# Performance work log

Measured on AMD Instinct MI355X. Metric: run time of the kernel, lower is better.

Reference implementation:

```python
import jax, jax.numpy as jnp
import numpy as np

BN_EPS = 1e-5
KNN_K = 9
HEAD = 4


def _bn(x, gamma, beta, axis=1):
    # eval-mode BatchNorm with running_mean=0, running_var=1
    shape = [1] * x.ndim
    shape[axis] = -1
    scale = (gamma / jnp.sqrt(1.0 + BN_EPS)).reshape(shape)
    return x * scale + beta.reshape(shape)


def _conv1d(x, W, b):
    # 1x1 Conv1d == channel matmul; x: [B,C,N], W: [O,C], b: [O]
    return jnp.einsum('oc,bcn->bon', W, x) + b[None, :, None]


def _knn_idx(x, k):
    # x: [B,C,N] -> idx [B,N,k] of k nearest (incl. self)
    xx = jnp.sum(x * x, axis=1)                      # [B,N]
    inner = jnp.einsum('bcn,bcm->bnm', x, x)         # [B,N,N]
    neg_d = 2.0 * inner - xx[:, :, None] - xx[:, None, :]
    return jax.lax.top_k(neg_d, k)[1]


def _graph_feature(x, k):
    # x: [B,C,N] -> [B,2C,N,k]  (cat of center feature and center - neighbor)
    B, C, N = x.shape
    idx = _knn_idx(x, k)                             # [B,N,k]
    xt = jnp.transpose(x, (0, 2, 1))                 # [B,N,C]
    nbr = jax.vmap(lambda xb, ib: xb[ib])(xt, idx)   # [B,N,k,C]
    ctr = jnp.broadcast_to(xt[:, :, None, :], (B, N, k, C))
    feat = jnp.concatenate([ctr, ctr - nbr], axis=3)  # [B,N,k,2C]
    return jnp.transpose(feat, (0, 3, 1, 2))


def _dgcnn_max(x, w1, b1, g1, be1, w2, b2, g2, be2, k):
    # x: [B,C,N] -> [B,C,N]; two 1x1 convs + BN + ReLU then max over k
    ef = _graph_feature(x, k)                        # [B,2C,N,k]
    h = jnp.einsum('oc,bcnk->bonk', w1, ef) + b1[None, :, None, None]
    h = jax.nn.relu(_bn(h, g1, be1, axis=1))
    h = jnp.einsum('oc,bcnk->bonk', w2, h) + b2[None, :, None, None]
    h = jax.nn.relu(_bn(h, g2, be2, axis=1))
    return jnp.max(h, axis=-1)                       # [B,C,N]


def _attention(m1, m2, wq, bq, wk, bk, wv, bv, wmh, bmh, wc1, bc1, cg, cbe, wc2, bc2):
    B, C, N = m1.shape
    hd = C // HEAD
    q = _conv1d(m1, wq, bq).reshape(B, HEAD, hd, N)
    kk = _conv1d(m2, wk, bk).reshape(B, HEAD, hd, -1)
    v = _conv1d(m2, wv, bv).reshape(B, HEAD, hd, -1)
    score = jax.nn.softmax(jnp.einsum('bhdn,bhdm->bhnm', q, kk) / (float(hd) ** 0.5), axis=-1)
    add = jnp.einsum('bhnm,bhdm->bhdn', score, v).reshape(B, C, N)
    add = _conv1d(add, wmh, bmh)
    cat = jnp.concatenate([m1, add], axis=1)         # [B,2C,N]
    h = jax.nn.relu(_bn(_conv1d(cat, wc1, bc1), cg, cbe, axis=1))
    return m1 + _conv1d(h, wc2, bc2)


def setup_inputs() -> dict:
    key = jax.random.key(0)
    B, C, N = 4, 128, 2000
    ks = jax.random.split(key, 24)

    def w(k, shape, s=0.05):
        return jax.random.normal(k, shape, dtype=jnp.float32) * s

    inp = {
        'x': jax.random.normal(ks[0], (B, C, N, 1), dtype=jnp.float32),
        'y': jax.random.normal(ks[1], (B, C, N), dtype=jnp.float32),
        # DGCNN_MAX_Block conv params (two 1x1 Conv2d + BN)
        'dg_w1': w(ks[2], (C, 2 * C)), 'dg_b1': w(ks[3], (C,)),
        'dg_g1': jnp.ones((C,), jnp.float32), 'dg_be1': jnp.zeros((C,), jnp.float32),
        'dg_w2': w(ks[4], (C, C)), 'dg_b2': w(ks[5], (C,)),
        'dg_g2': jnp.ones((C,), jnp.float32), 'dg_be2': jnp.zeros((C,), jnp.float32),
        # AttentionPropagation params
        'wq': w(ks[6], (C, C)), 'bq': w(ks[7], (C,)),
        'wk': w(ks[8], (C, C)), 'bk': w(ks[9], (C,)),
        'wv': w(ks[10], (C, C)), 'bv': w(ks[11], (C,)),
        'wmh': w(ks[12], (C, C)), 'bmh': w(ks[13], (C,)),
        'wc1': w(ks[14], (2 * C, 2 * C)), 'bc1': w(ks[15], (2 * C,)),
        'cg': jnp.ones((2 * C,), jnp.float32), 'cbe': jnp.zeros((2 * C,), jnp.float32),
        'wc2': w(ks[16], (C, 2 * C)), 'bc2': w(ks[17], (C,)),
    }
    return inp


def reference(x, y, dg_w1, dg_b1, dg_g1, dg_be1, dg_w2, dg_b2, dg_g2, dg_be2,
              wq, bq, wk, bk, wv, bv, wmh, bmh, wc1, bc1, cg, cbe, wc2, bc2):
    feats = x[:, :, :, 0]                            # [B,C,N]
    agg = _dgcnn_max(feats, dg_w1, dg_b1, dg_g1, dg_be1,
                     dg_w2, dg_b2, dg_g2, dg_be2, KNN_K)
    out = _attention(agg, y, wq, bq, wk, bk, wv, bv, wmh, bmh,
                     wc1, bc1, cg, cbe, wc2, bc2)
    return out[:, :, :, None]                        # [B,C,N,1]
```

## Files before the change

### kernel.cpp

```cpp
#include <hip/hip_runtime.h>

#define BATCH 4
#define CH    128
#define NPTS  2000
#define KNN   9
#define NHEAD 4
#define HD    32
#define NHALF 1000

typedef unsigned short u16;
typedef __attribute__((ext_vector_type(4))) float f32x4;
typedef __attribute__((ext_vector_type(8))) short bf16x8;

#define OFF_XT    0
#define OFF_YT    1024000
#define OFF_PT    2048000
#define OFF_QT    3072000
#define OFF_AGG   4096000
#define OFF_MH    5120000
#define OFF_MISC  6144000
#define OFF_W1SUM (OFF_MISC)
#define OFF_W1B   (OFF_MISC+16384)
#define OFF_W2T   (OFF_MISC+32768)
#define OFF_ML0   (OFF_MISC+49152)
#define OFF_WC1T  (OFF_MISC+114688)
#define OFF_B1F   (OFF_MISC+212992)
#define OFF_B2F   (OFF_MISC+213120)
#define OFF_BC1F  (OFF_MISC+213248)
#define OFF_XX    (OFF_MISC+213504)
#define OFF_IDX   (OFF_MISC+221504)

__device__ __forceinline__ void bsplit(float v, u16& hi, u16& lo)
{
    unsigned u = __float_as_uint(v);
    unsigned h16 = (u + 0x7fffu + ((u >> 16) & 1u)) >> 16;
    float hf = __uint_as_float(h16 << 16);
    float lf = v - hf;
    unsigned ul = __float_as_uint(lf);
    hi = (u16)h16;
    lo = (u16)((ul + 0x7fffu + ((ul >> 16) & 1u)) >> 16);
}

__device__ __forceinline__ f32x4 mfma16(bf16x8 a, bf16x8 b, f32x4 c)
{
    return __builtin_amdgcn_mfma_f32_16x16x32_bf16(a, b, c, 0, 0, 0);
}

__global__ __launch_bounds__(256) void prep_kernel(
    const float* __restrict__ w1, const float* __restrict__ b1,
    const float* __restrict__ g1, const float* __restrict__ be1,
    const float* __restrict__ w2, const float* __restrict__ b2,
    const float* __restrict__ g2, const float* __restrict__ be2,
    const float* __restrict__ wc1, const float* __restrict__ bc1,
    const float* __restrict__ cg, const float* __restrict__ cbe,
    float* __restrict__ ws)
{
    int id = blockIdx.x * 256 + threadIdx.x;
    const float rs = rsqrtf(1.f + 1e-5f);
    if (id < 16384) {
        int o = id >> 7;
        int c = id & 127;
        float s1 = g1[o] * rs;
        ws[OFF_W1SUM + id] = (w1[o*256 + c] + w1[o*256 + 128 + c]) * s1;
        ws[OFF_W1B   + id] = w1[o*256 + 128 + c] * s1;
        ws[OFF_W2T   + id] = w2[id] * (g2[o] * rs);
    }
    {
        int o = id >> 8;
        ws[OFF_WC1T + id] = wc1[id] * (cg[o] * rs);
    }
    if (id < 128) {
        float s1 = g1[id] * rs, s2 = g2[id] * rs;
        ws[OFF_B1F + id] = b1[id]*s1 + be1[id];
        ws[OFF_B2F + id] = b2[id]*s2 + be2[id];
    }
    if (id < 256) {
        ws[OFF_BC1F + id] = bc1[id]*(cg[id]*rs) + cbe[id];
    }
}

__global__ __launch_bounds__(128) void transpose_split_kernel(
    const float* __restrict__ src, float* __restrict__ dst, float* __restrict__ xx,
    u16* __restrict__ H, u16* __restrict__ L)
{
    int blk = blockIdx.x; int b = blk / NPTS, n = blk % NPTS;
    int c = threadIdx.x;
    float v = src[((size_t)b*CH + c)*NPTS + n];
    size_t di = ((size_t)b*NPTS + n)*CH + c;
    dst[di] = v;
    u16 hi, lo;
    bsplit(v, hi, lo);
    H[di] = hi; L[di] = lo;
    __shared__ float red[128];
    red[c] = v*v;
    __syncthreads();
    for (int s = 64; s > 0; s >>= 1) { if (c < s) red[c] += red[c+s]; __syncthreads(); }
    if (c == 0) xx[b*NPTS + n] = red[0];
}

__global__ __launch_bounds__(128) void transpose_kernel(
    const float* __restrict__ src, float* __restrict__ dst)
{
    int blk = blockIdx.x; int b = blk / NPTS, n = blk % NPTS;
    int c = threadIdx.x;
    dst[((size_t)b*NPTS + n)*CH + c] = src[((size_t)b*CH + c)*NPTS + n];
}

__global__ __launch_bounds__(512) void knn8_kernel(
    const u16* __restrict__ XH, const u16* __restrict__ XL,
    const float* __restrict__ xx, int* __restrict__ idxOut)
{
    __shared__ float woutv[8][16][9];
    __shared__ int   wouti[8][16][9];
    int b = blockIdx.y;
    int q0 = blockIdx.x * 16;
    int tid = threadIdx.x;
    int wave = tid >> 6, lane = tid & 63;
    int lg = lane >> 4, lr = lane & 15;
    const float* xxb = xx + (size_t)b*NPTS;

    size_t qb = ((size_t)b*NPTS + q0 + lr)*128 + lg*8;
    bf16x8 qh[4], ql[4];
#pragma unroll
    for (int ch = 0; ch < 4; ch++) {
        qh[ch] = *(const bf16x8*)&XH[qb + ch*32];
        ql[ch] = *(const bf16x8*)&XL[qb + ch*32];
    }

    float vals[4][9]; int ids[4][9];
    float vmin[4]; int amin[4];
#pragma unroll
    for (int j = 0; j < 4; j++) {
#pragma unroll
        for (int k = 0; k < 9; k++) { vals[j][k] = -3.4e38f; ids[j][k] = -1; }
        vmin[j] = -3.4e38f; amin[j] = 0;
    }

    for (int t = wave; t < 125; t += 8) {
        size_t kb = ((size_t)b*NPTS + t*16 + lr)*128 + lg*8;
        bf16x8 fh[4], fl[4];
#pragma unroll
        for (int ch = 0; ch < 4; ch++) {
            fh[ch] = *(const bf16x8*)&XH[kb + ch*32];
            fl[ch] = *(const bf16x8*)&XL[kb + ch*32];
        }
        float xv = xxb[t*16 + lr];
        f32x4 acc = {0.f,0.f,0.f,0.f};
#pragma unroll
        for (int ch = 0; ch < 4; ch++) {
            acc = mfma16(qh[ch], fh[ch], acc);
            acc = mfma16(qh[ch], fl[ch], acc);
            acc = mfma16(ql[ch], fh[ch], acc);
            acc = mfma16(ql[ch], fl[ch], acc);
        }
        int cand = t*16 + lr;
#pragma unroll
        for (int j = 0; j < 4; j++) {
            float s = 2.f*acc[j] - xv;
            if (s > vmin[j]) {
#pragma unroll
                for (int k = 0; k < 9; k++) {
                    bool sel = (k == amin[j]);
                    vals[j][k] = sel ? s    : vals[j][k];
                    ids[j][k]  = sel ? cand : ids[j][k];
                }
                vmin[j] = vals[j][0]; amin[j] = 0;
#pragma unroll
                for (int k = 1; k < 9; k++) {
                    bool lt = vals[j][k] < vmin[j];
                    vmin[j] = lt ? vals[j][k] : vmin[j];
                    amin[j] = lt ? k : amin[j];
                }
            }
        }
    }

#pragma unroll
    for (int j = 0; j < 4; j++) {
        unsigned used = 0;
        for (int r = 0; r < 9; r++) {
            float bv = -3.4e38f; int bm = -1;
#pragma unroll
            for (int k = 0; k < 9; k++) {
                bool ok = !(used & (1u << k)) && (vals[j][k] > bv);
                bv = ok ? vals[j][k] : bv;
                bm = ok ? ids[j][k]  : bm;
            }
            float v = bv; int mi = bm;
#pragma unroll
            for (int off = 1; off < 16; off <<= 1) {
                float ov = __shfl_xor(v, off);
                int  omi = __shfl_xor(mi, off);
                if (ov > v || (ov == v && omi >= 0 && omi < mi)) { v = ov; mi = omi; }
            }
#pragma unroll
            for (int k = 0; k < 9; k++) {
                if (ids[j][k] == mi) used |= (1u << k);
            }
            if (lr == 0) { woutv[wave][lg*4+j][r] = v; wouti[wave][lg*4+j][r] = mi; }
        }
    }
    __syncthreads();

    if (tid < 16) {
        float v0 = woutv[0][tid][0], v1 = woutv[1][tid][0], v2 = woutv[2][tid][0], v3 = woutv[3][tid][0];
        float v4 = woutv[4][tid][0], v5 = woutv[5][tid][0], v6 = woutv[6][tid][0], v7 = woutv[7][tid][0];
        int   i0 = wouti[0][tid][0], i1 = wouti[1][tid][0], i2 = wouti[2][tid][0], i3 = wouti[3][tid][0];
        int   i4 = wouti[4][tid][0], i5 = wouti[5][tid][0], i6 = wouti[6][tid][0], i7 = wouti[7][tid][0];
        int   p0 = 1, p1 = 1, p2 = 1, p3 = 1, p4 = 1, p5 = 1, p6 = 1, p7 = 1;
        int* op = idxOut + ((size_t)b*NPTS + q0 + tid)*KNN;
        for (int r = 0; r < 9; r++) {
            int w = 0; float bv = v0; int bi = i0;
            if (v1 > bv || (v1 == bv && i1 < bi)) { w = 1; bv = v1; bi = i1; }
            if (v2 > bv || (v2 == bv && i2 < bi)) { w = 2; bv = v2; bi = i2; }
            if (v3 > bv || (v3 == bv && i3 < bi)) { w = 3; bv = v3; bi = i3; }
            if (v4 > bv || (v4 == bv && i4 < bi)) { w = 4; bv = v4; bi = i4; }
            if (v5 > bv || (v5 == bv && i5 < bi)) { w = 5; bv = v5; bi = i5; }
            if (v6 > bv || (v6 == bv && i6 < bi)) { w = 6; bv = v6; bi = i6; }
            if (v7 > bv || (v7 == bv && i7 < bi)) { w = 7; bv = v7; bi = i7; }
            op[r] = bi;
            if (w == 0)      { v0 = (p0 < 9) ? woutv[0][tid][p0] : -3.4e38f; i0 = (p0 < 9) ? wouti[0][tid][p0] : 0x7fffffff; p0++; }
            else if (w == 1) { v1 = (p1 < 9) ? woutv[1][tid][p1] : -3.4e38f; i1 = (p1 < 9) ? wouti[1][tid][p1] : 0x7fffffff; p1++; }
            else if (w == 2) { v2 = (p2 < 9) ? woutv[2][tid][p2] : -3.4e38f; i2 = (p2 < 9) ? wouti[2][tid][p2] : 0x7fffffff; p2++; }
            else if (w == 3) { v3 = (p3 < 9) ? woutv[3][tid][p3] : -3.4e38f; i3 = (p3 < 9) ? wouti[3][tid][p3] : 0x7fffffff; p3++; }
            else if (w == 4) { v4 = (p4 < 9) ? woutv[4][tid][p4] : -3.4e38f; i4 = (p4 < 9) ? wouti[4][tid][p4] : 0x7fffffff; p4++; }
            else if (w == 5) { v5 = (p5 < 9) ? woutv[5][tid][p5] : -3.4e38f; i5 = (p5 < 9) ? wouti[5][tid][p5] : 0x7fffffff; p5++; }
            else if (w == 6) { v6 = (p6 < 9) ? woutv[6][tid][p6] : -3.4e38f; i6 = (p6 < 9) ? wouti[6][tid][p6] : 0x7fffffff; p6++; }
            else             { v7 = (p7 < 9) ? woutv[7][tid][p7] : -3.4e38f; i7 = (p7 < 9) ? wouti[7][tid][p7] : 0x7fffffff; p7++; }
        }
    }
}

__global__ __launch_bounds__(128) void gemm_dual_kernel(
    const float* __restrict__ In, const float* __restrict__ Wa, const float* __restrict__ Wb,
    const float* __restrict__ ba, const float* __restrict__ bb,
    float* __restrict__ OutA, float* __restrict__ OutB)
{
    __shared__ float in_lds[8][128];
    int row0 = blockIdx.x * 8, tid = threadIdx.x;
    const float* src = In + (size_t)row0 * 128;
    for (int i = tid; i < 1024; i += 128) ((float*)in_lds)[i] = src[i];
    __syncthreads();
    float accA[8], accB[8];
    float bA = ba ? ba[tid] : 0.f, bB = bb ? bb[tid] : 0.f;
#pragma unroll
    for (int j = 0; j < 8; j++) { accA[j] = bA; accB[j] = bB; }
    const float4* wra = (const float4*)(Wa + (size_t)tid * 128);
    const float4* wrb = (const float4*)(Wb + (size_t)tid * 128);
#pragma unroll 4
    for (int c4 = 0; c4 < 32; c4++) {
        float4 wa = wra[c4], wb = wrb[c4];
#pragma unroll
        for (int j = 0; j < 8; j++) {
            float4 xi = ((const float4*)&in_lds[j][0])[c4];
            accA[j] += xi.x*wa.x + xi.y*wa.y + xi.z*wa.z + xi.w*wa.w;
            accB[j] += xi.x*wb.x + xi.y*wb.y + xi.z*wb.z + xi.w*wb.w;
        }
    }
#pragma unroll
    for (int j = 0; j < 8; j++) {
        OutA[(size_t)(row0 + j)*128 + tid] = accA[j];
        OutB[(size_t)(row0 + j)*128 + tid] = accB[j];
    }
}

__global__ __launch_bounds__(128) void gemm_kv_kernel(
    const float* __restrict__ In, const float* __restrict__ Wa, const float* __restrict__ Wb,
    const float* __restrict__ ba, const float* __restrict__ bb,
    u16* __restrict__ KHo, u16* __restrict__ KLo,
    u16* __restrict__ VTHo, u16* __restrict__ VTLo)
{
    __shared__ float in_lds[8][128];
    int row0 = blockIdx.x * 8, tid = threadIdx.x;
    const float* src = In + (size_t)row0 * 128;
    for (int i = tid; i < 1024; i += 128) ((float*)in_lds)[i] = src[i];
    __syncthreads();
    float accA[8], accB[8];
    float bA = ba[tid], bB = bb[tid];
#pragma unroll
    for (int j = 0; j < 8; j++) { accA[j] = bA; accB[j] = bB; }
    const float4* wra = (const float4*)(Wa + (size_t)tid * 128);
    const float4* wrb = (const float4*)(Wb + (size_t)tid * 128);
#pragma unroll 4
    for (int c4 = 0; c4 < 32; c4++) {
        float4 wa = wra[c4], wb = wrb[c4];
#pragma unroll
        for (int j = 0; j < 8; j++) {
            float4 xi = ((const float4*)&in_lds[j][0])[c4];
            accA[j] += xi.x*wa.x + xi.y*wa.y + xi.z*wa.z + xi.w*wa.w;
            accB[j] += xi.x*wb.x + xi.y*wb.y + xi.z*wb.z + xi.w*wb.w;
        }
    }
    int b = row0 / NPTS, n0 = row0 % NPTS;
#pragma unroll
    for (int j = 0; j < 8; j++) {
        u16 hh, ll;
        bsplit(accA[j], hh, ll);
        size_t ko = (size_t)(row0 + j)*128 + tid;
        KHo[ko] = hh; KLo[ko] = ll;
        bsplit(accB[j], hh, ll);
        size_t vo = ((size_t)b*128 + tid)*NPTS + n0 + j;
        VTHo[vo] = hh; VTLo[vo] = ll;
    }
}

__global__ __launch_bounds__(128) void gemm_q_kernel(
    const float* __restrict__ In, const float* __restrict__ Wt, const float* __restrict__ bias,
    u16* __restrict__ H, u16* __restrict__ L)
{
    __shared__ float in_lds[8][128];
    int row0 = blockIdx.x * 8, tid = threadIdx.x;
    const float* src = In + (size_t)row0 * 128;
    for (int i = tid; i < 1024; i += 128) ((float*)in_lds)[i] = src[i];
    __syncthreads();
    float acc[8];
    float b = bias[tid];
#pragma unroll
    for (int j = 0; j < 8; j++) acc[j] = b;
    const float4* wrow = (const float4*)(Wt + (size_t)tid * 128);
#pragma unroll 4
    for (int c4 = 0; c4 < 32; c4++) {
        float4 w = wrow[c4];
#pragma unroll
        for (int j = 0; j < 8; j++) {
            float4 xi = ((const float4*)&in_lds[j][0])[c4];
            acc[j] += xi.x*w.x + xi.y*w.y + xi.z*w.z + xi.w*w.w;
        }
    }
#pragma unroll
    for (int j = 0; j < 8; j++) {
        u16 hh, ll;
        bsplit(acc[j], hh, ll);
        size_t o = (size_t)(row0 + j)*128 + tid;
        H[o] = hh; L[o] = ll;
    }
}

template<int CIN, int COUT, bool RELU, bool TRANSOUT, bool HASRES, bool CONCAT>
__global__ __launch_bounds__(COUT) void gemmT_kernel(
    const float* __restrict__ In, const float* __restrict__ In2,
    const float* __restrict__ Wt, const float* __restrict__ bias,
    const float* __restrict__ Res, float* __restrict__ Out)
{
    __shared__ float in_lds[8][CIN];
    int row0 = blockIdx.x * 8, tid = threadIdx.x;
    if (!CONCAT) {
        const float* src = In + (size_t)row0 * CIN;
        for (int i = tid; i < 8*CIN; i += COUT) ((float*)in_lds)[i] = src[i];
    } else {
        for (int i = tid; i < 8*128; i += COUT) {
            int j = i >> 7, c = i & 127;
            in_lds[j][c]       = In [(size_t)(row0 + j)*128 + c];
            in_lds[j][128 + c] = In2[(size_t)(row0 + j)*128 + c];
        }
    }
    __syncthreads();
    float acc[8];
    float b = bias ? bias[tid] : 0.f;
#pragma unroll
    for (int j = 0; j < 8; j++) acc[j] = b;
    const float4* wrow = (const float4*)(Wt + (size_t)tid * CIN);
#pragma unroll 4
    for (int c4 = 0; c4 < CIN/4; c4++) {
        float4 w = wrow[c4];
#pragma unroll
        for (int j = 0; j < 8; j++) {
            float4 xi = ((const float4*)&in_lds[j][0])[c4];
            acc[j] += xi.x*w.x + xi.y*w.y + xi.z*w.z + xi.w*w.w;
        }
    }
#pragma unroll
    for (int j = 0; j < 8; j++) {
        float v = acc[j];
        if (RELU) v = fmaxf(v, 0.f);
        size_t row = row0 + j;
        if (HASRES) v += Res[row*COUT + tid];
        if (!TRANSOUT) {
            Out[row*COUT + tid] = v;
        } else {
            int b_ = (int)(row / NPTS), n_ = (int)(row % NPTS);
            Out[((size_t)b_*COUT + tid)*NPTS + n_] = v;
        }
    }
}

__global__ __launch_bounds__(128) void edgeconv_kernel(
    const float* __restrict__ Pt, const float* __restrict__ Qt,
    const int* __restrict__ idx, const float* __restrict__ W2t,
    const float* __restrict__ b2f, float* __restrict__ Agg)
{
    int blk = blockIdx.x; int b = blk / NPTS, n = blk % NPTS;
    int o = threadIdx.x;
    __shared__ float r[9][128];
    __shared__ int mk[9];
    if (o < 9) mk[o] = idx[((size_t)b*NPTS + n)*KNN + o];
    __syncthreads();
    float p = Pt[((size_t)b*NPTS + n)*128 + o];
#pragma unroll
    for (int k = 0; k < 9; k++) {
        float q = Qt[((size_t)b*NPTS + mk[k])*128 + o];
        r[k][o] = fmaxf(p - q, 0.f);
    }
    __syncthreads();
    float acc[9];
#pragma unroll
    for (int k = 0; k < 9; k++) acc[k] = 0.f;
    const float4* w2row = (const float4*)(W2t + (size_t)o * 128);
#pragma unroll 2
    for (int c4 = 0; c4 < 32; c4++) {
        float4 w = w2row[c4];
#pragma unroll
        for (int k = 0; k < 9; k++) {
            float4 rv = ((const float4*)&r[k][0])[c4];
            acc[k] += rv.x*w.x + rv.y*w.y + rv.z*w.z + rv.w*w.w;
        }
    }
    float bb = b2f[o];
    float vmax = -3.4e38f;
#pragma unroll
    for (int k = 0; k < 9; k++) vmax = fmaxf(vmax, fmaxf(acc[k] + bb, 0.f));
    Agg[((size_t)b*NPTS + n)*128 + o] = vmax;
}

#define PSTR 72
__global__ __launch_bounds__(256) void attn_mfma_kernel(
    const u16* __restrict__ QH, const u16* __restrict__ QL,
    const u16* __restrict__ KH, const u16* __restrict__ KL,
    const u16* __restrict__ VTH, const u16* __restrict__ VTL,
    float* __restrict__ O0, float* __restrict__ O1,
    float* __restrict__ ML0, float* __restrict__ ML1)
{
    __shared__ alignas(16) u16 Ph[4][16][PSTR];
    __shared__ alignas(16) u16 Pl[4][16][PSTR];
    int b = blockIdx.z, h = blockIdx.y;
    int split = blockIdx.x & 1, qt = blockIdx.x >> 1;
    int wave = threadIdx.x >> 6, lane = threadIdx.x & 63;
    int lg = lane >> 4, lr = lane & 15;
    int q0 = qt * 64 + wave * 16;
    if (q0 >= NPTS) return;
    int kstart = split * NHALF, kend = kstart + NHALF;
    float* Op = split ? O1 : O0;
    float* ml = split ? ML1 : ML0;

    size_t qb = ((size_t)b*NPTS + q0 + lr)*128 + h*32 + lg*8;
    const bf16x8 qh = *(const bf16x8*)&QH[qb];
    const bf16x8 ql = *(const bf16x8*)&QL[qb];

    f32x4 o0 = {0.f,0.f,0.f,0.f}, o1 = {0.f,0.f,0.f,0.f};
    float mrun[4], lsum[4];
#pragma unroll
    for (int r = 0; r < 4; r++) { mrun[r] = -3.0e38f; lsum[r] = 0.f; }
    const float sc = 0.17677669529663687f;
    int shsrc = ((lr >> 2) << 4) | (lr & 3);

    for (int ks = kstart; ks < kend; ks += 32) {
        int k0i = ks + lr;      bool vk0 = k0i < kend; if (k0i > kend-1) k0i = kend-1;
        int k1i = ks + 16 + lr; bool vk1 = k1i < kend; if (k1i > kend-1) k1i = kend-1;
        size_t kb0 = ((size_t)b*NPTS + k0i)*128 + h*32 + lg*8;
        size_t kb1 = ((size_t)b*NPTS + k1i)*128 + h*32 + lg*8;
        bf16x8 k0h = *(const bf16x8*)&KH[kb0];
        bf16x8 k0l = *(const bf16x8*)&KL[kb0];
        bf16x8 k1h = *(const bf16x8*)&KH[kb1];
        bf16x8 k1l = *(const bf16x8*)&KL[kb1];
        f32x4 s0 = {0.f,0.f,0.f,0.f}, s1 = {0.f,0.f,0.f,0.f};
        s0 = mfma16(qh, k0h, s0);
        s0 = mfma16(qh, k0l, s0);
        s0 = mfma16(ql, k0h, s0);
        s1 = mfma16(qh, k1h, s1);
        s1 = mfma16(qh, k1l, s1);
        s1 = mfma16(ql, k1h, s1);
        float mx[4];
#pragma unroll
        for (int r = 0; r < 4; r++) {
            float a  = vk0 ? s0[r]*sc : -3.0e38f;
            float a2 = vk1 ? s1[r]*sc : -3.0e38f;
            s0[r] = a; s1[r] = a2;
            mx[r] = fmaxf(a, a2);
        }
#pragma unroll
        for (int off = 1; off < 16; off <<= 1) {
#pragma unroll
            for (int r = 0; r < 4; r++) mx[r] = fmaxf(mx[r], __shfl_xor(mx[r], off));
        }
        float e0[4], e1[4], rsu[4], sca[4];
#pragma unroll
        for (int r = 0; r < 4; r++) {
            float mn = fmaxf(mrun[r], mx[r]);
            sca[r] = __expf(mrun[r] - mn);
            mrun[r] = mn;
            e0[r] = __expf(s0[r] - mn);
            e1[r] = __expf(s1[r] - mn);
            rsu[r] = e0[r] + e1[r];
        }
#pragma unroll
        for (int off = 1; off < 16; off <<= 1) {
#pragma unroll
            for (int r = 0; r < 4; r++) rsu[r] += __shfl_xor(rsu[r], off);
        }
#pragma unroll
        for (int r = 0; r < 4; r++) lsum[r] = lsum[r]*sca[r] + rsu[r];
#pragma unroll
        for (int r = 0; r < 4; r++) {
            u16 h0, w0, h1, w1;
            bsplit(e0[r], h0, w0);
            bsplit(e1[r], h1, w1);
            int qr = lg*4 + r;
            Ph[wave][qr][lr]      = h0;
            Pl[wave][qr][lr]      = w0;
            Ph[wave][qr][16 + lr] = h1;
            Pl[wave][qr][16 + lr] = w1;
        }
        float scsel = (lr & 2) ? ((lr & 1) ? sca[3] : sca[2])
                               : ((lr & 1) ? sca[1] : sca[0]);
        float osc = __shfl(scsel, shsrc);
#pragma unroll
        for (int r = 0; r < 4; r++) { o0[r] *= osc; o1[r] *= osc; }
        int cb = ks + lg*8; if (cb > kend-8) cb = kend-8;
        bf16x8 pbh = *(const bf16x8*)&Ph[wave][lr][lg*8];
        bf16x8 pbl = *(const bf16x8*)&Pl[wave][lr][lg*8];
        size_t vb = ((size_t)b*128 + h*32 + lr)*NPTS + cb;
        bf16x8 v0h = *(const bf16x8*)&VTH[vb];
        bf16x8 v0l = *(const bf16x8*)&VTL[vb];
        bf16x8 v1h = *(const bf16x8*)&VTH[vb + 16*NPTS];
        bf16x8 v1l = *(const bf16x8*)&VTL[vb + 16*NPTS];
        o0 = mfma16(v0h, pbh, o0);
        o0 = mfma16(v0l, pbh, o0);
        o0 = mfma16(v0h, pbl, o0);
        o1 = mfma16(v1h, pbh, o1);
        o1 = mfma16(v1l, pbh, o1);
        o1 = mfma16(v1h, pbl, o1);
    }
    if (lr == 0) {
#pragma unroll
        for (int r = 0; r < 4; r++) {
            size_t mo = (((size_t)b*NHEAD + h)*NPTS + q0 + lg*4 + r)*2;
            ml[mo]   = mrun[r];
            ml[mo+1] = lsum[r];
        }
    }
    int q = q0 + lr;
    size_t ob = ((size_t)b*NPTS + q)*128 + h*32;
#pragma unroll
    for (int r = 0; r < 4; r++) {
        Op[ob + lg*4 + r]      = o0[r];
        Op[ob + 16 + lg*4 + r] = o1[r];
    }
}

__global__ __launch_bounds__(256) void attn_merge_kernel(
    const float* __restrict__ O0, const float* __restrict__ ML0,
    const float* __restrict__ ML1, float* __restrict__ O1 )
{
    int id = blockIdx.x * 256 + threadIdx.x;
    int c = id & 127;
    int q = (id >> 7) % NPTS;
    int b = id / (NPTS * 128);
    int h = c >> 5;
    size_t mo = (((size_t)b*NHEAD + h)*NPTS + q)*2;
    float m0 = ML0[mo], l0 = ML0[mo+1];
    float m1 = ML1[mo], l1 = ML1[mo+1];
    float M = fmaxf(m0, m1);
    float w0 = __expf(m0 - M), w1 = __expf(m1 - M);
    float inv = 1.f / (l0*w0 + l1*w1);
    O1[id] = (O0[id]*w0 + O1[id]*w1) * inv;
}

extern "C" void kernel_launch(void* const* d_in, const int* in_sizes, int n_in,
                              void* d_out, int out_size, void* d_ws, size_t ws_size,
                              hipStream_t stream)
{
    const float* x    = (const float*)d_in[0];
    const float* y    = (const float*)d_in[1];
    const float* w1   = (const float*)d_in[2];
    const float* b1   = (const float*)d_in[3];
    const float* g1   = (const float*)d_in[4];
    const float* be1  = (const float*)d_in[5];
    const float* w2   = (const float*)d_in[6];
    const float* b2   = (const float*)d_in[7];
    const float* g2   = (const float*)d_in[8];
    const float* be2  = (const float*)d_in[9];
    const float* wq   = (const float*)d_in[10];
    const float* bq   = (const float*)d_in[11];
    const float* wk   = (const float*)d_in[12];
    const float* bk   = (const float*)d_in[13];
    const float* wv   = (const float*)d_in[14];
    const float* bv   = (const float*)d_in[15];
    const float* wmh  = (const float*)d_in[16];
    const float* bmh  = (const float*)d_in[17];
    const float* wc1  = (const float*)d_in[18];
    const float* bc1  = (const float*)d_in[19];
    const float* cg   = (const float*)d_in[20];
    const float* cbe  = (const float*)d_in[21];
    const float* wc2  = (const float*)d_in[22];
    const float* bc2  = (const float*)d_in[23];
    float* ws = (float*)d_ws;
    float* out = (float*)d_out;

    float* XT  = ws + OFF_XT;
    float* YT  = ws + OFF_YT;
    float* PT  = ws + OFF_PT;
    float* QT  = ws + OFF_QT;
    float* AGG = ws + OFF_AGG;
    float* MH  = ws + OFF_MH;
    float* XX  = ws + OFF_XX;
    int*   IDX = (int*)(ws + OFF_IDX);
    float* O0s = XT;
    float* O1s = YT;
    float* ADD = YT;
    float* ML0 = ws + OFF_ML0;
    float* ML1 = ws + OFF_XX;
    float* TT  = PT;
    const int SPE = BATCH*NPTS*CH;
    u16* XHs = (u16*)MH;  u16* XLs = XHs + SPE;
    u16* QHs = (u16*)MH;  u16* QLs = QHs + SPE;
    u16* KHs = (u16*)QT;  u16* KLs = KHs + SPE;
    u16* VTH = (u16*)PT;  u16* VTL = VTH + SPE;

    prep_kernel<<<256, 256, 0, stream>>>(w1, b1, g1, be1, w2, b2, g2, be2,
                                         wc1, bc1, cg, cbe, ws);
    transpose_split_kernel<<<BATCH*NPTS, 128, 0, stream>>>(x, XT, XX, XHs, XLs);
    transpose_kernel<<<BATCH*NPTS, 128, 0, stream>>>(y, YT);
    knn8_kernel<<<dim3(NPTS/16, BATCH), 512, 0, stream>>>(XHs, XLs, XX, IDX);
    gemm_dual_kernel<<<BATCH*NPTS/8, 128, 0, stream>>>(XT, ws + OFF_W1SUM, ws + OFF_W1B,
                                                       ws + OFF_B1F, nullptr, PT, QT);
    edgeconv_kernel<<<BATCH*NPTS, 128, 0, stream>>>(PT, QT, IDX, ws + OFF_W2T,
                                                    ws + OFF_B2F, AGG);
    gemm_q_kernel<<<BATCH*NPTS/8, 128, 0, stream>>>(AGG, wq, bq, QHs, QLs);
    gemm_kv_kernel<<<BATCH*NPTS/8, 128, 0, stream>>>(YT, wk, wv, bk, bv,
                                                     KHs, KLs, VTH, VTL);
    attn_mfma_kernel<<<dim3(64, NHEAD, BATCH), 256, 0, stream>>>(
        QHs, QLs, KHs, KLs, VTH, VTL, O0s, O1s, ML0, ML1);
    attn_merge_kernel<<<BATCH*NPTS*CH/256, 256, 0, stream>>>(O0s, ML0, ML1, O1s);
    gemmT_kernel<128,128,false,false,false,false><<<BATCH*NPTS/8, 128, 0, stream>>>(
        ADD, nullptr, wmh, bmh, nullptr, MH);
    gemmT_kernel<256,256,true,false,false,true><<<BATCH*NPTS/8, 256, 0, stream>>>(
        AGG, MH, ws + OFF_WC1T, ws + OFF_BC1F, nullptr, TT);
    gemmT_kernel<256,128,false,true,true,false><<<BATCH*NPTS/8, 128, 0, stream>>>(
        TT, nullptr, wc2, bc2, AGG, out);
}
```

Measured before the change: 539.9 us.

## Split KNN candidate range across two blocks and merge partial top-k lists

The KNN kernel now launches a third grid dimension that splits the candidate tiles into two halves. Each block writes its sorted partial top-9 values and indices to scratch space inside the AGG buffer. A new merge kernel then combines the two lists per query into the final indices. This doubles the block count (125x4 was only 500 blocks) to use more of the GPU, at the cost of an extra launch, duplicated query loads, and scratch traffic.

```diff
diff --git a/kernel.cpp b/kernel.cpp
--- a/kernel.cpp
+++ b/kernel.cpp
@@ -108,16 +108,19 @@
 
 __global__ __launch_bounds__(512) void knn8_kernel(
     const u16* __restrict__ XH, const u16* __restrict__ XL,
-    const float* __restrict__ xx, int* __restrict__ idxOut)
+    const float* __restrict__ xx, float* __restrict__ PV, int* __restrict__ PI)
 {
     __shared__ float woutv[8][16][9];
     __shared__ int   wouti[8][16][9];
     int b = blockIdx.y;
+    int half = blockIdx.z;
     int q0 = blockIdx.x * 16;
     int tid = threadIdx.x;
     int wave = tid >> 6, lane = tid & 63;
     int lg = lane >> 4, lr = lane & 15;
     const float* xxb = xx + (size_t)b*NPTS;
+    int tstart = half ? 63 : 0;
+    int tend   = half ? 125 : 63;
 
     size_t qb = ((size_t)b*NPTS + q0 + lr)*128 + lg*8;
     bf16x8 qh[4], ql[4];
@@ -136,7 +139,7 @@
         vmin[j] = -3.4e38f; amin[j] = 0;
     }
 
-    for (int t = wave; t < 125; t += 8) {
+    for (int t = tstart + wave; t < tend; t += 8) {
         size_t kb = ((size_t)b*NPTS + t*16 + lr)*128 + lg*8;
         bf16x8 fh[4], fl[4];
 #pragma unroll
@@ -208,7 +211,7 @@
         int   i0 = wouti[0][tid][0], i1 = wouti[1][tid][0], i2 = wouti[2][tid][0], i3 = wouti[3][tid][0];
         int   i4 = wouti[4][tid][0], i5 = wouti[5][tid][0], i6 = wouti[6][tid][0], i7 = wouti[7][tid][0];
         int   p0 = 1, p1 = 1, p2 = 1, p3 = 1, p4 = 1, p5 = 1, p6 = 1, p7 = 1;
-        int* op = idxOut + ((size_t)b*NPTS + q0 + tid)*KNN;
+        size_t po = (((size_t)half*BATCH + b)*NPTS + q0 + tid)*9;
         for (int r = 0; r < 9; r++) {
             int w = 0; float bv = v0; int bi = i0;
             if (v1 > bv || (v1 == bv && i1 < bi)) { w = 1; bv = v1; bi = i1; }
@@ -218,7 +221,7 @@
             if (v5 > bv || (v5 == bv && i5 < bi)) { w = 5; bv = v5; bi = i5; }
             if (v6 > bv || (v6 == bv && i6 < bi)) { w = 6; bv = v6; bi = i6; }
             if (v7 > bv || (v7 == bv && i7 < bi)) { w = 7; bv = v7; bi = i7; }
-            op[r] = bi;
+            PV[po + r] = bv; PI[po + r] = bi;
             if (w == 0)      { v0 = (p0 < 9) ? woutv[0][tid][p0] : -3.4e38f; i0 = (p0 < 9) ? wouti[0][tid][p0] : 0x7fffffff; p0++; }
             else if (w == 1) { v1 = (p1 < 9) ? woutv[1][tid][p1] : -3.4e38f; i1 = (p1 < 9) ? wouti[1][tid][p1] : 0x7fffffff; p1++; }
             else if (w == 2) { v2 = (p2 < 9) ? woutv[2][tid][p2] : -3.4e38f; i2 = (p2 < 9) ? wouti[2][tid][p2] : 0x7fffffff; p2++; }
@@ -228,6 +231,27 @@
             else if (w == 6) { v6 = (p6 < 9) ? woutv[6][tid][p6] : -3.4e38f; i6 = (p6 < 9) ? wouti[6][tid][p6] : 0x7fffffff; p6++; }
             else             { v7 = (p7 < 9) ? woutv[7][tid][p7] : -3.4e38f; i7 = (p7 < 9) ? wouti[7][tid][p7] : 0x7fffffff; p7++; }
         }
+    }
+}
+
+__global__ __launch_bounds__(256) void knn_merge_kernel(
+    const float* __restrict__ PV, const int* __restrict__ PI, int* __restrict__ idxOut)
+{
+    int q = blockIdx.x * 256 + threadIdx.x;
+    if (q >= BATCH*NPTS) return;
+    const float* v0p = PV + (size_t)q*9;
+    const int*   i0p = PI + (size_t)q*9;
+    const float* v1p = PV + ((size_t)BATCH*NPTS + q)*9;
+    const int*   i1p = PI + ((size_t)BATCH*NPTS + q)*9;
+    int p0 = 0, p1 = 0;
+    int* op = idxOut + (size_t)q*9;
+#pragma unroll
+    for (int r = 0; r < 9; r++) {
+        float a = v0p[p0], bb = v1p[p1];
+        int ia = i0p[p0], ib = i1p[p1];
+        bool takeB = (bb > a) || (bb == a && ib < ia);
+        op[r] = takeB ? ib : ia;
+        if (takeB) p1++; else p0++;
     }
 }
 
@@ -610,6 +634,8 @@
     float* ML0 = ws + OFF_ML0;
     float* ML1 = ws + OFF_XX;
     float* TT  = PT;
+    float* KPV = AGG;
+    int*   KPI = (int*)(AGG + 144000);
     const int SPE = BATCH*NPTS*CH;
     u16* XHs = (u16*)MH;  u16* XLs = XHs + SPE;
     u16* QHs = (u16*)MH;  u16* QLs = QHs + SPE;
@@ -620,7 +646,8 @@
                                          wc1, bc1, cg, cbe, ws);
     transpose_split_kernel<<<BATCH*NPTS, 128, 0, stream>>>(x, XT, XX, XHs, XLs);
     transpose_kernel<<<BATCH*NPTS, 128, 0, stream>>>(y, YT);
-    knn8_kernel<<<dim3(NPTS/16, BATCH), 512, 0, stream>>>(XHs, XLs, XX, IDX);
+    knn8_kernel<<<dim3(NPTS/16, BATCH, 2), 512, 0, stream>>>(XHs, XLs, XX, KPV, KPI);
+    knn_merge_kernel<<<(BATCH*NPTS + 255)/256, 256, 0, stream>>>(KPV, KPI, IDX);
     gemm_dual_kernel<<<BATCH*NPTS/8, 128, 0, stream>>>(XT, ws + OFF_W1SUM, ws + OFF_W1B,
                                                        ws + OFF_B1F, nullptr, PT, QT);
     edgeconv_kernel<<<BATCH*NPTS, 128, 0, stream>>>(PT, QT, IDX, ws + OFF_W2T,
```

Result: slower. 594.4 us (+10.1%).
